# Kernel tuning notes

Measured on AMD Instinct MI355X. Metric: run time of the kernel, lower is better.

Reference implementation:

```python
import jax, jax.numpy as jnp
import numpy as np

DIM = 768
N_HEADS = 12
HEAD_DIM = DIM // N_HEADS
HIDDEN = int(DIM * 4.0)
EPS = 1e-6


def setup_inputs() -> dict:
    key = jax.random.key(0)
    ks = jax.random.split(key, 12)
    s = 0.02
    return {
        "x": jax.random.normal(ks[0], (4, 2048, DIM), dtype=jnp.float32),
        "ln1_g": jnp.ones((DIM,), jnp.float32),
        "ln1_b": jnp.zeros((DIM,), jnp.float32),
        "qkv_w": jax.random.normal(ks[1], (3 * DIM, DIM), jnp.float32) * s,
        "qkv_b": jnp.zeros((3 * DIM,), jnp.float32),
        "proj_w": jax.random.normal(ks[2], (DIM, DIM), jnp.float32) * s,
        "proj_b": jnp.zeros((DIM,), jnp.float32),
        "ln2_g": jnp.ones((DIM,), jnp.float32),
        "ln2_b": jnp.zeros((DIM,), jnp.float32),
        "fc1_w": jax.random.normal(ks[3], (HIDDEN, DIM), jnp.float32) * s,
        "fc1_b": jnp.zeros((HIDDEN,), jnp.float32),
        "fc2_w": jax.random.normal(ks[4], (DIM, HIDDEN), jnp.float32) * s,
        "fc2_b": jnp.zeros((DIM,), jnp.float32),
    }


def layer_norm(x, g, b):
    mu = jnp.mean(x, axis=-1, keepdims=True)
    var = jnp.mean(jnp.square(x - mu), axis=-1, keepdims=True)
    return (x - mu) * jax.lax.rsqrt(var + EPS) * g + b


def reference(x, ln1_g, ln1_b, qkv_w, qkv_b, proj_w, proj_b,
              ln2_g, ln2_b, fc1_w, fc1_b, fc2_w, fc2_b):
    B, N, D = x.shape
    # --- attention branch ---
    h = layer_norm(x, ln1_g, ln1_b)
    qkv = h @ qkv_w.T + qkv_b                      # [B, N, 3D]
    qkv = qkv.reshape(B, N, 3, N_HEADS, HEAD_DIM).transpose(2, 0, 3, 1, 4)
    q, k, v = qkv[0], qkv[1], qkv[2]               # each [B, H, N, d]
    scale = HEAD_DIM ** -0.5
    scores = jnp.einsum("bhqd,bhkd->bhqk", q, k) * scale
    attn = jax.nn.softmax(scores, axis=-1)
    out = jnp.einsum("bhqk,bhkd->bhqd", attn, v)   # [B, H, N, d]
    out = out.transpose(0, 2, 1, 3).reshape(B, N, D)
    x = x + (out @ proj_w.T + proj_b)
    # --- MLP branch ---
    h = layer_norm(x, ln2_g, ln2_b)
    h = jax.nn.gelu(h @ fc1_w.T + fc1_b, approximate=False)
    x = x + (h @ fc2_w.T + fc2_b)
    return x
```

## Files before the change

kernel.cpp:

```cpp
#include <hip/hip_runtime.h>


#define DIM    768
#define NHEAD  12
#define HDIM   64
#define HID    3072
#define BATCH  4
#define SEQ    2048
#define MTOT   (BATCH * SEQ)
#define D3     (3 * DIM)

#define QSCALE 0.18033688011112042f
#define GELU_K 2.30220816f

typedef short bf16x8 __attribute__((ext_vector_type(8)));
typedef float f32x4  __attribute__((ext_vector_type(4)));

__device__ __forceinline__ float exp2fast(float x) {
    return __builtin_amdgcn_exp2f(x);
}

__device__ __forceinline__ float gelu_f(float v) {
    float y = v * (1.f + 0.044715f * v * v) * GELU_K;
    float t = exp2fast(fminf(y, 30.f));
#if __has_builtin(__builtin_amdgcn_rcpf)
    return v * t * __builtin_amdgcn_rcpf(t + 1.f);
#else
    return v * t / (t + 1.f);
#endif
}

__device__ __forceinline__ short f2bf(float f) {
    union { float f; unsigned u; } c; c.f = f;
    unsigned r = c.u + 0x7FFFu + ((c.u >> 16) & 1u);
    return (short)(r >> 16);
}

__device__ __forceinline__ short4 pk4bf(float a, float b, float c, float d) {
    int lo, hi;
    asm("v_cvt_pk_bf16_f32 %0, %1, %2" : "=v"(lo) : "v"(a), "v"(b));
    asm("v_cvt_pk_bf16_f32 %0, %1, %2" : "=v"(hi) : "v"(c), "v"(d));
    short4 r;
    *(int*)&r.x = lo; *(int*)&r.z = hi;
    return r;
}

__device__ __forceinline__ void gld_lds16(const short* g, short* l) {
    __builtin_amdgcn_global_load_lds(
        (const __attribute__((address_space(1))) unsigned int*)g,
        (__attribute__((address_space(3))) unsigned int*)l, 16, 0, 0);
}

__global__ __launch_bounds__(256) void tobf4_k(
    const float* __restrict__ s0, short* __restrict__ d0, int n0,
    const float* __restrict__ s1, short* __restrict__ d1, int n1,
    const float* __restrict__ s2, short* __restrict__ d2, int n2,
    const float* __restrict__ s3, short* __restrict__ d3, int n3)
{
    int i = blockIdx.x * 256 + threadIdx.x;
    const float* s; short* d;
    if (i < n0)                { s = s0; d = d0; }
    else if ((i -= n0) < n1)   { s = s1; d = d1; }
    else if ((i -= n1) < n2)   { s = s2; d = d2; }
    else if ((i -= n2) < n3)   { s = s3; d = d3; }
    else return;
    float4 v = ((const float4*)s)[i];
    ((short4*)d)[i] = pk4bf(v.x, v.y, v.z, v.w);
}

__global__ __launch_bounds__(256) void ln_k(
    const float* __restrict__ x, const float* __restrict__ g,
    const float* __restrict__ bta, short* __restrict__ y)
{
    __shared__ float sb[2][4];
    const int row = blockIdx.x, tid = threadIdx.x;
    const float* xr = x + (size_t)row * DIM;
    float v0 = xr[tid], v1 = xr[tid + 256], v2 = xr[tid + 512];
    float s = v0 + v1 + v2;
    #pragma unroll
    for (int o = 32; o; o >>= 1) s += __shfl_down(s, o);
    if ((tid & 63) == 0) sb[0][tid >> 6] = s;
    __syncthreads();
    float mu = (sb[0][0] + sb[0][1] + sb[0][2] + sb[0][3]) * (1.f / DIM);
    float d0 = v0 - mu, d1 = v1 - mu, d2 = v2 - mu;
    float q = d0 * d0 + d1 * d1 + d2 * d2;
    #pragma unroll
    for (int o = 32; o; o >>= 1) q += __shfl_down(q, o);
    if ((tid & 63) == 0) sb[1][tid >> 6] = q;
    __syncthreads();
    float var = (sb[1][0] + sb[1][1] + sb[1][2] + sb[1][3]) * (1.f / DIM);
    float inv = rsqrtf(var + 1e-6f);
    short* yr = y + (size_t)row * DIM;
    yr[tid]       = f2bf(d0 * inv * g[tid]       + bta[tid]);
    yr[tid + 256] = f2bf(d1 * inv * g[tid + 256] + bta[tid + 256]);
    yr[tid + 512] = f2bf(d2 * inv * g[tid + 512] + bta[tid + 512]);
}

template<int MODE>
__global__ __launch_bounds__(512) void gemm8_k(
    const short* __restrict__ A, const short* __restrict__ W,
    const float* __restrict__ bias, const float* __restrict__ resid,
    void* __restrict__ Cout, short* __restrict__ vt,
    int M, int N, int K)
{
    __shared__ __align__(16) short sm[2][24576];

    const int tid = threadIdx.x, lane = tid & 63, wv = tid >> 6;
    const int l15 = lane & 15, quad = lane >> 4;
    const int bm = blockIdx.y << 8, bn = blockIdx.x << 7;

    const int srow  = lane >> 3;
    const int chunk = (lane & 7) ^ srow;
    const int arow  = wv * 8 + srow;

    const short* Ag = A + (size_t)(bm + arow) * K + chunk * 8;
    const short* Wg = W + (size_t)(bn + arow) * K + chunk * 8;

    const int nt = K >> 6;

    auto stage = [&](short* s, int k0) {
        #pragma unroll
        for (int u = 0; u < 2; ++u)
            #pragma unroll
            for (int i = 0; i < 2; ++i)
                gld_lds16(Ag + k0 + (size_t)(u * 128 + i * 64) * K,
                          s + u * 8192 + i * 4096 + wv * 512);
        #pragma unroll
        for (int i = 0; i < 2; ++i)
            gld_lds16(Wg + k0 + (size_t)(i * 64) * K,
                      s + 16384 + i * 4096 + wv * 512);
    };

    f32x4 acc[4][4] = {};
    stage(&sm[0][0], 0);

    const int rsel = (wv >> 1) * 64;
    const int csel = (wv & 1) * 64;
    const int xorr = (l15 & 7) << 4;

    for (int t = 0; t < nt; ++t) {
        const short* Sc = &sm[t & 1][0];
        asm volatile("s_waitcnt vmcnt(0)" ::: "memory");
        __builtin_amdgcn_s_barrier();
        __builtin_amdgcn_sched_barrier(0);
        const int kn = (t + 1 < nt ? t + 1 : t) << 6;
        stage(&sm[(t + 1) & 1][0], kn);

        #pragma unroll
        for (int ks = 0; ks < 2; ++ks) {
            bf16x8 af[4], bfr[4];
            #pragma unroll
            for (int mf = 0; mf < 4; ++mf) {
                const int row = rsel + mf * 16 + l15;
                const int off = (row >> 7) * 16384 + ((row & 127) << 7)
                              + (((ks << 6) + (quad << 4)) ^ xorr);
                af[mf] = *(const bf16x8*)((const char*)Sc + off);
            }
            #pragma unroll
            for (int nf = 0; nf < 4; ++nf) {
                const int brow = csel + nf * 16 + l15;
                const int off = 32768 + (brow << 7)
                              + (((ks << 6) + (quad << 4)) ^ xorr);
                bfr[nf] = *(const bf16x8*)((const char*)Sc + off);
            }
            __builtin_amdgcn_s_setprio(1);
            #pragma unroll
            for (int mf = 0; mf < 4; ++mf)
                #pragma unroll
                for (int nf = 0; nf < 4; ++nf)
                    acc[mf][nf] = __builtin_amdgcn_mfma_f32_16x16x32_bf16(
                        af[mf], bfr[nf], acc[mf][nf], 0, 0, 0);
            __builtin_amdgcn_s_setprio(0);
        }
    }

    if (MODE == 3 && bn >= 1536) {
        const size_t bbase = (size_t)(bm >> 11) * NHEAD;
        #pragma unroll
        for (int nf = 0; nf < 4; ++nf) {
            const int col = bn + csel + nf * 16 + l15;
            const float bv = bias[col];
            const int d = col - 1536, hh = d >> 6, dd = d & 63;
            const size_t vrow = (((bbase + hh) << 6) + dd) * SEQ;
            #pragma unroll
            for (int mf = 0; mf < 4; ++mf) {
                const int n0 = (bm & 2047) + rsel + mf * 16 + (quad << 2);
                *(short4*)&vt[vrow + n0] =
                    pk4bf(acc[mf][nf][0] + bv, acc[mf][nf][1] + bv,
                          acc[mf][nf][2] + bv, acc[mf][nf][3] + bv);
            }
        }
        return;
    }

    #pragma unroll
    for (int nf = 0; nf < 4; ++nf) {
        const int col = bn + csel + nf * 16 + l15;
        const float bv = bias[col];
        #pragma unroll
        for (int mf = 0; mf < 4; ++mf) {
            const int row0 = bm + rsel + mf * 16 + (quad << 2);
            #pragma unroll
            for (int r = 0; r < 4; ++r) {
                float v = acc[mf][nf][r] + bv;
                const size_t idx = (size_t)(row0 + r) * N + col;
                if (MODE == 0) {
                    ((float*)Cout)[idx] = v + resid[idx];
                } else if (MODE == 2) {
                    ((short*)Cout)[idx] = f2bf(gelu_f(v));
                } else {
                    if (col < DIM) v *= QSCALE;
                    ((short*)Cout)[idx] = f2bf(v);
                }
            }
        }
    }
}

__global__ __launch_bounds__(256) void attn_k(
    const short* __restrict__ qkv, const short* __restrict__ vt,
    short* __restrict__ out)
{
    __shared__ __align__(16) short Ks[64][72];
    __shared__ __align__(16) short Vs[64][72];
    __shared__ __align__(16) short Ps[4][32][72];

    const int bh = blockIdx.x, b = bh / NHEAD, h = bh % NHEAD;
    const int qb = blockIdx.y;
    const int tid = threadIdx.x, lane = tid & 63, wv = tid >> 6;
    const int l15 = lane & 15, quad = lane >> 4;

    const size_t qbase = (size_t)b * SEQ * D3;
    const size_t vbase = (((size_t)bh) << 6) * SEQ;

    bf16x8 qf[2][2];
    #pragma unroll
    for (int tm = 0; tm < 2; ++tm) {
        const int m = (qb << 7) + wv * 32 + tm * 16 + l15;
        #pragma unroll
        for (int ks = 0; ks < 2; ++ks)
            qf[tm][ks] = *(const bf16x8*)&qkv[qbase + (size_t)m * D3 + h * HDIM
                                             + ks * 32 + (quad << 3)];
    }

    float psum[2] = {0.f, 0.f};
    f32x4 acc[2][4] = {};

    const int srow = tid >> 3;
    const int scol = (tid & 7) << 3;

    for (int kb = 0; kb < SEQ / 64; ++kb) {
        __syncthreads();
        #pragma unroll
        for (int p = 0; p < 2; ++p) {
            const int r = srow + p * 32;
            *(int4*)&Ks[r][scol] = *(const int4*)&qkv[qbase
                + (size_t)((kb << 6) + r) * D3 + DIM + h * HDIM + scol];
            *(int4*)&Vs[r][scol] = *(const int4*)&vt[vbase
                + (size_t)r * SEQ + (kb << 6) + scol];
        }
        __syncthreads();

        f32x4 st[2][4] = {};
        #pragma unroll
        for (int kt = 0; kt < 4; ++kt)
            #pragma unroll
            for (int ks = 0; ks < 2; ++ks) {
                bf16x8 kf = *(const bf16x8*)&Ks[kt * 16 + l15][ks * 32 + (quad << 3)];
                #pragma unroll
                for (int tm = 0; tm < 2; ++tm)
                    st[tm][kt] = __builtin_amdgcn_mfma_f32_16x16x32_bf16(
                        kf, qf[tm][ks], st[tm][kt], 0, 0, 0);
            }

        #pragma unroll
        for (int tm = 0; tm < 2; ++tm) {
            #pragma unroll
            for (int kt = 0; kt < 4; ++kt) {
                const float p0 = exp2fast(st[tm][kt][0]);
                const float p1 = exp2fast(st[tm][kt][1]);
                const float p2 = exp2fast(st[tm][kt][2]);
                const float p3 = exp2fast(st[tm][kt][3]);
                psum[tm] += (p0 + p1) + (p2 + p3);
                *(short4*)&Ps[wv][tm * 16 + l15][kt * 16 + (quad << 2)] =
                    pk4bf(p0, p1, p2, p3);
            }
        }

        #pragma unroll
        for (int ks = 0; ks < 2; ++ks) {
            bf16x8 pf[2];
            #pragma unroll
            for (int tm = 0; tm < 2; ++tm)
                pf[tm] = *(const bf16x8*)&Ps[wv][tm * 16 + l15][ks * 32 + (quad << 3)];
            #pragma unroll
            for (int u = 0; u < 4; ++u) {
                bf16x8 vf = *(const bf16x8*)&Vs[u * 16 + l15][ks * 32 + (quad << 3)];
                #pragma unroll
                for (int tm = 0; tm < 2; ++tm)
                    acc[tm][u] = __builtin_amdgcn_mfma_f32_16x16x32_bf16(
                        vf, pf[tm], acc[tm][u], 0, 0, 0);
            }
        }
    }

    #pragma unroll
    for (int tm = 0; tm < 2; ++tm) {
        psum[tm] += __shfl_xor(psum[tm], 16);
        psum[tm] += __shfl_xor(psum[tm], 32);
    }

    #pragma unroll
    for (int tm = 0; tm < 2; ++tm) {
        const float inv = 1.f / psum[tm];
        const int q = (qb << 7) + wv * 32 + tm * 16 + l15;
        #pragma unroll
        for (int u = 0; u < 4; ++u) {
            const int d0 = u * 16 + (quad << 2);
            *(short4*)&out[((size_t)b * SEQ + q) * DIM + h * HDIM + d0] =
                pk4bf(acc[tm][u][0] * inv, acc[tm][u][1] * inv,
                      acc[tm][u][2] * inv, acc[tm][u][3] * inv);
        }
    }
}

extern "C" void kernel_launch(void* const* d_in, const int* in_sizes, int n_in,
                              void* d_out, int out_size, void* d_ws, size_t ws_size,
                              hipStream_t stream) {
    const float* x      = (const float*)d_in[0];
    const float* ln1_g  = (const float*)d_in[1];
    const float* ln1_b  = (const float*)d_in[2];
    const float* qkv_w  = (const float*)d_in[3];
    const float* qkv_b  = (const float*)d_in[4];
    const float* proj_w = (const float*)d_in[5];
    const float* proj_b = (const float*)d_in[6];
    const float* ln2_g  = (const float*)d_in[7];
    const float* ln2_b  = (const float*)d_in[8];
    const float* fc1_w  = (const float*)d_in[9];
    const float* fc1_b  = (const float*)d_in[10];
    const float* fc2_w  = (const float*)d_in[11];
    const float* fc2_b  = (const float*)d_in[12];
    float* out = (float*)d_out;

    short* ws16 = (short*)d_ws;
    short* wqkv = ws16;
    short* wprj = wqkv + (size_t)D3 * DIM;
    short* wf1  = wprj + (size_t)DIM * DIM;
    short* wf2  = wf1  + (size_t)HID * DIM;
    short* h    = wf2  + (size_t)DIM * HID;
    short* big  = h    + (size_t)MTOT * DIM;
    short* vtb  = big  + (size_t)MTOT * HID;
    float* x2   = (float*)(vtb + (size_t)MTOT * DIM);

    dim3 blk(256);

    const int n0 = (D3 * DIM) / 4, n1 = (DIM * DIM) / 4,
              n2 = (HID * DIM) / 4, n3 = (DIM * HID) / 4;
    tobf4_k<<<(n0 + n1 + n2 + n3 + 255) / 256, blk, 0, stream>>>(
        qkv_w, wqkv, n0, proj_w, wprj, n1, fc1_w, wf1, n2, fc2_w, wf2, n3);

    ln_k<<<MTOT, blk, 0, stream>>>(x, ln1_g, ln1_b, h);
    gemm8_k<3><<<dim3(D3 / 128, MTOT / 256), 512, 0, stream>>>(
        h, wqkv, qkv_b, nullptr, big, vtb, MTOT, D3, DIM);
    attn_k<<<dim3(BATCH * NHEAD, SEQ / 128), blk, 0, stream>>>(big, vtb, h);
    gemm8_k<0><<<dim3(DIM / 128, MTOT / 256), 512, 0, stream>>>(
        h, wprj, proj_b, x, x2, nullptr, MTOT, DIM, DIM);
    ln_k<<<MTOT, blk, 0, stream>>>(x2, ln2_g, ln2_b, vtb);
    gemm8_k<2><<<dim3(HID / 128, MTOT / 256), 512, 0, stream>>>(
        vtb, wf1, fc1_b, nullptr, big, nullptr, MTOT, HID, DIM);
    gemm8_k<0><<<dim3(DIM / 128, MTOT / 256), 512, 0, stream>>>(
        big, wf2, fc2_b, x2, out, nullptr, MTOT, DIM, HID);
}
```

Baseline: 391.3 us.

## Retile GEMMs to 128x192 with triple-buffered LDS and swizzle attention LDS

The GEMM tile changes from 256x128 to 128x192 with a 2x4 wave layout, and the single-stage double buffer becomes a three-buffer pipeline that waits on vmcnt(5), so two K tiles are in flight at once. Launch grids are resized to match. The attention kernel drops its padded LDS rows in favour of XOR-swizzled 64-wide rows for K, V and P, aiming to avoid bank conflicts with less LDS. Risks include a different arithmetic-intensity balance, since N=768 splits into only 4 column blocks, and a more delicate wait-count correctness with the new staging.

```diff
diff --git a/kernel.cpp b/kernel.cpp
--- a/kernel.cpp
+++ b/kernel.cpp
@@ -103,11 +103,12 @@
     void* __restrict__ Cout, short* __restrict__ vt,
     int M, int N, int K)
 {
-    __shared__ __align__(16) short sm[2][24576];
+    __shared__ __align__(16) short sm[3][20480];
 
     const int tid = threadIdx.x, lane = tid & 63, wv = tid >> 6;
     const int l15 = lane & 15, quad = lane >> 4;
-    const int bm = blockIdx.y << 8, bn = blockIdx.x << 7;
+    const int bm = blockIdx.y << 7;
+    const int bn = blockIdx.x * 192;
 
     const int srow  = lane >> 3;
     const int chunk = (lane & 7) ^ srow;
@@ -120,54 +121,50 @@
 
     auto stage = [&](short* s, int k0) {
         #pragma unroll
-        for (int u = 0; u < 2; ++u)
-            #pragma unroll
-            for (int i = 0; i < 2; ++i)
-                gld_lds16(Ag + k0 + (size_t)(u * 128 + i * 64) * K,
-                          s + u * 8192 + i * 4096 + wv * 512);
-        #pragma unroll
         for (int i = 0; i < 2; ++i)
+            gld_lds16(Ag + k0 + (size_t)(i * 64) * K,
+                      s + i * 4096 + wv * 512);
+        #pragma unroll
+        for (int i = 0; i < 3; ++i)
             gld_lds16(Wg + k0 + (size_t)(i * 64) * K,
-                      s + 16384 + i * 4096 + wv * 512);
+                      s + 8192 + i * 4096 + wv * 512);
     };
 
-    f32x4 acc[4][4] = {};
+    f32x4 acc[4][3] = {};
     stage(&sm[0][0], 0);
-
-    const int rsel = (wv >> 1) * 64;
-    const int csel = (wv & 1) * 64;
+    stage(&sm[1][0], (nt > 1 ? 1 : 0) << 6);
+
+    const int rsel = (wv >> 2) * 64;
+    const int csel = (wv & 3) * 48;
     const int xorr = (l15 & 7) << 4;
 
     for (int t = 0; t < nt; ++t) {
-        const short* Sc = &sm[t & 1][0];
-        asm volatile("s_waitcnt vmcnt(0)" ::: "memory");
+        const char* Sc = (const char*)&sm[t % 3][0];
+        asm volatile("s_waitcnt vmcnt(5)" ::: "memory");
         __builtin_amdgcn_s_barrier();
         __builtin_amdgcn_sched_barrier(0);
-        const int kn = (t + 1 < nt ? t + 1 : t) << 6;
-        stage(&sm[(t + 1) & 1][0], kn);
+        const int kn = (t + 2 < nt ? t + 2 : nt - 1) << 6;
+        stage(&sm[(t + 2) % 3][0], kn);
 
         #pragma unroll
         for (int ks = 0; ks < 2; ++ks) {
-            bf16x8 af[4], bfr[4];
+            bf16x8 af[4], bfr[3];
+            const int kc = ((ks << 6) + (quad << 4)) ^ xorr;
             #pragma unroll
             for (int mf = 0; mf < 4; ++mf) {
                 const int row = rsel + mf * 16 + l15;
-                const int off = (row >> 7) * 16384 + ((row & 127) << 7)
-                              + (((ks << 6) + (quad << 4)) ^ xorr);
-                af[mf] = *(const bf16x8*)((const char*)Sc + off);
-            }
-            #pragma unroll
-            for (int nf = 0; nf < 4; ++nf) {
+                af[mf] = *(const bf16x8*)(Sc + (row << 7) + kc);
+            }
+            #pragma unroll
+            for (int nf = 0; nf < 3; ++nf) {
                 const int brow = csel + nf * 16 + l15;
-                const int off = 32768 + (brow << 7)
-                              + (((ks << 6) + (quad << 4)) ^ xorr);
-                bfr[nf] = *(const bf16x8*)((const char*)Sc + off);
+                bfr[nf] = *(const bf16x8*)(Sc + 16384 + (brow << 7) + kc);
             }
             __builtin_amdgcn_s_setprio(1);
             #pragma unroll
             for (int mf = 0; mf < 4; ++mf)
                 #pragma unroll
-                for (int nf = 0; nf < 4; ++nf)
+                for (int nf = 0; nf < 3; ++nf)
                     acc[mf][nf] = __builtin_amdgcn_mfma_f32_16x16x32_bf16(
                         af[mf], bfr[nf], acc[mf][nf], 0, 0, 0);
             __builtin_amdgcn_s_setprio(0);
@@ -177,7 +174,7 @@
     if (MODE == 3 && bn >= 1536) {
         const size_t bbase = (size_t)(bm >> 11) * NHEAD;
         #pragma unroll
-        for (int nf = 0; nf < 4; ++nf) {
+        for (int nf = 0; nf < 3; ++nf) {
             const int col = bn + csel + nf * 16 + l15;
             const float bv = bias[col];
             const int d = col - 1536, hh = d >> 6, dd = d & 63;
@@ -194,7 +191,7 @@
     }
 
     #pragma unroll
-    for (int nf = 0; nf < 4; ++nf) {
+    for (int nf = 0; nf < 3; ++nf) {
         const int col = bn + csel + nf * 16 + l15;
         const float bv = bias[col];
         #pragma unroll
@@ -221,14 +218,15 @@
     const short* __restrict__ qkv, const short* __restrict__ vt,
     short* __restrict__ out)
 {
-    __shared__ __align__(16) short Ks[64][72];
-    __shared__ __align__(16) short Vs[64][72];
-    __shared__ __align__(16) short Ps[4][32][72];
+    __shared__ __align__(16) short Ks[64][64];
+    __shared__ __align__(16) short Vs[64][64];
+    __shared__ __align__(16) short Ps[4][32][64];
 
     const int bh = blockIdx.x, b = bh / NHEAD, h = bh % NHEAD;
     const int qb = blockIdx.y;
     const int tid = threadIdx.x, lane = tid & 63, wv = tid >> 6;
     const int l15 = lane & 15, quad = lane >> 4;
+    const int lsw = (l15 & 7) << 3;
 
     const size_t qbase = (size_t)b * SEQ * D3;
     const size_t vbase = (((size_t)bh) << 6) * SEQ;
@@ -254,9 +252,10 @@
         #pragma unroll
         for (int p = 0; p < 2; ++p) {
             const int r = srow + p * 32;
-            *(int4*)&Ks[r][scol] = *(const int4*)&qkv[qbase
+            const int pc = scol ^ ((r & 7) << 3);
+            *(int4*)&Ks[r][pc] = *(const int4*)&qkv[qbase
                 + (size_t)((kb << 6) + r) * D3 + DIM + h * HDIM + scol];
-            *(int4*)&Vs[r][scol] = *(const int4*)&vt[vbase
+            *(int4*)&Vs[r][pc] = *(const int4*)&vt[vbase
                 + (size_t)r * SEQ + (kb << 6) + scol];
         }
         __syncthreads();
@@ -266,7 +265,8 @@
         for (int kt = 0; kt < 4; ++kt)
             #pragma unroll
             for (int ks = 0; ks < 2; ++ks) {
-                bf16x8 kf = *(const bf16x8*)&Ks[kt * 16 + l15][ks * 32 + (quad << 3)];
+                bf16x8 kf = *(const bf16x8*)
+                    &Ks[kt * 16 + l15][(ks * 32 + (quad << 3)) ^ lsw];
                 #pragma unroll
                 for (int tm = 0; tm < 2; ++tm)
                     st[tm][kt] = __builtin_amdgcn_mfma_f32_16x16x32_bf16(
@@ -282,7 +282,8 @@
                 const float p2 = exp2fast(st[tm][kt][2]);
                 const float p3 = exp2fast(st[tm][kt][3]);
                 psum[tm] += (p0 + p1) + (p2 + p3);
-                *(short4*)&Ps[wv][tm * 16 + l15][kt * 16 + (quad << 2)] =
+                *(short4*)&Ps[wv][tm * 16 + l15]
+                             [(kt * 16 + (quad << 2)) ^ lsw] =
                     pk4bf(p0, p1, p2, p3);
             }
         }
@@ -292,10 +293,12 @@
             bf16x8 pf[2];
             #pragma unroll
             for (int tm = 0; tm < 2; ++tm)
-                pf[tm] = *(const bf16x8*)&Ps[wv][tm * 16 + l15][ks * 32 + (quad << 3)];
+                pf[tm] = *(const bf16x8*)
+                    &Ps[wv][tm * 16 + l15][(ks * 32 + (quad << 3)) ^ lsw];
             #pragma unroll
             for (int u = 0; u < 4; ++u) {
-                bf16x8 vf = *(const bf16x8*)&Vs[u * 16 + l15][ks * 32 + (quad << 3)];
+                bf16x8 vf = *(const bf16x8*)
+                    &Vs[u * 16 + l15][(ks * 32 + (quad << 3)) ^ lsw];
                 #pragma unroll
                 for (int tm = 0; tm < 2; ++tm)
                     acc[tm][u] = __builtin_amdgcn_mfma_f32_16x16x32_bf16(
@@ -360,14 +363,14 @@
         qkv_w, wqkv, n0, proj_w, wprj, n1, fc1_w, wf1, n2, fc2_w, wf2, n3);
 
     ln_k<<<MTOT, blk, 0, stream>>>(x, ln1_g, ln1_b, h);
-    gemm8_k<3><<<dim3(D3 / 128, MTOT / 256), 512, 0, stream>>>(
+    gemm8_k<3><<<dim3(D3 / 192, MTOT / 128), 512, 0, stream>>>(
         h, wqkv, qkv_b, nullptr, big, vtb, MTOT, D3, DIM);
     attn_k<<<dim3(BATCH * NHEAD, SEQ / 128), blk, 0, stream>>>(big, vtb, h);
-    gemm8_k<0><<<dim3(DIM / 128, MTOT / 256), 512, 0, stream>>>(
+    gemm8_k<0><<<dim3(DIM / 192, MTOT / 128), 512, 0, stream>>>(
         h, wprj, proj_b, x, x2, nullptr, MTOT, DIM, DIM);
     ln_k<<<MTOT, blk, 0, stream>>>(x2, ln2_g, ln2_b, vtb);
-    gemm8_k<2><<<dim3(HID / 128, MTOT / 256), 512, 0, stream>>>(
+    gemm8_k<2><<<dim3(HID / 192, MTOT / 128), 512, 0, stream>>>(
         vtb, wf1, fc1_b, nullptr, big, nullptr, MTOT, HID, DIM);
-    gemm8_k<0><<<dim3(DIM / 128, MTOT / 256), 512, 0, stream>>>(
+    gemm8_k<0><<<dim3(DIM / 192, MTOT / 128), 512, 0, stream>>>(
         big, wf2, fc2_b, x2, out, nullptr, MTOT, DIM, HID);
 }
```

Result: faster. 378.3 us (-3.3%).
